# Optimization experiments

Hardware: AMD Instinct MI355X
Metric: run time of the kernel (lower is better)

Reference implementation:

```python
import jax, jax.numpy as jnp
import numpy as np

B, L, HID = 128, 256, 768
HID2 = 2 * HID
CDIM, SDIM, NPROJ = 192, 128, 128
FDIM = CDIM + SDIM + 1
BIG = 1e9  # finite pad so sorted invalid tokens go last without inf/nan issues


def setup_inputs() -> dict:
    key = jax.random.key(0)
    ks = jax.random.split(key, 12)
    H = jax.random.normal(ks[0], (B, L, HID), dtype=jnp.float32)
    tt = jax.random.randint(ks[1], (B, L), 0, 2, dtype=jnp.int32)
    m = jnp.ones((B, L), dtype=jnp.int32)
    s = 1.0 / np.sqrt(HID2)
    Wc = jax.random.uniform(ks[2], (CDIM, HID2), minval=-s, maxval=s, dtype=jnp.float32)
    bc = jax.random.uniform(ks[3], (CDIM,), minval=-s, maxval=s, dtype=jnp.float32)
    Ws = jax.random.uniform(ks[4], (SDIM, HID2), minval=-s, maxval=s, dtype=jnp.float32)
    bs = jax.random.uniform(ks[5], (SDIM,), minval=-s, maxval=s, dtype=jnp.float32)
    gate = jnp.array([0.5], dtype=jnp.float32)
    ln_g = jnp.ones((FDIM,), dtype=jnp.float32)
    ln_b = jnp.zeros((FDIM,), dtype=jnp.float32)
    sc = 1.0 / np.sqrt(FDIM)
    Wcls = jax.random.uniform(ks[6], (2, FDIM), minval=-sc, maxval=sc, dtype=jnp.float32)
    bcls = jax.random.uniform(ks[7], (2,), minval=-sc, maxval=sc, dtype=jnp.float32)
    d = jax.random.normal(ks[8], (NPROJ, HID), dtype=jnp.float32)
    proj_dirs = d / jnp.linalg.norm(d, axis=1, keepdims=True)
    return {"H": H, "tt": tt, "m": m, "Wc": Wc, "bc": bc, "Ws": Ws, "bs": bs,
            "gate": gate, "ln_g": ln_g, "ln_b": ln_b, "Wcls": Wcls, "bcls": bcls,
            "proj_dirs": proj_dirs}


def _forward(H, tt, m, Wc, bc, Ws, bs, gate, ln_g, ln_b, Wcls, bcls, proj_dirs):
    mask0 = (tt == 0) & (m == 1)  # [B,L]
    mask1 = (tt == 1) & (m == 1)
    f0 = mask0.astype(H.dtype)
    f1 = mask1.astype(H.dtype)
    cls = H[:, 0]  # [B,HID]
    mean0 = jnp.einsum('blh,bl->bh', H, f0) / jnp.clip(f0.sum(1, keepdims=True), 1.0)
    mean1 = jnp.einsum('blh,bl->bh', H, f1) / jnp.clip(f1.sum(1, keepdims=True), 1.0)
    rep = jnp.concatenate([cls, mean0 - mean1], axis=1)  # [B,2*HID]
    C = rep @ Wc.T + bc
    S = rep @ Ws.T + bs
    g = jax.nn.sigmoid(gate)  # [1]
    fused = jnp.concatenate([C * (1.0 - g), S * g], axis=1)

    # max-sliced W1 between token-type-0 and token-type-1 token sets, batched.
    P = jnp.einsum('blh,ph->blp', H, proj_dirs)  # [B,L,NPROJ]
    x0 = jnp.sort(jnp.where(mask0[..., None], P, BIG), axis=1)  # valid tokens first
    x1 = jnp.sort(jnp.where(mask1[..., None], P, BIG), axis=1)
    n0 = mask0.sum(1)
    n1 = mask1.sum(1)
    mcnt = jnp.minimum(n0, n1)  # [B]
    rmask = (jnp.arange(L)[None, :] < mcnt[:, None])[..., None]  # [B,L,1]
    diff = jnp.where(rmask, x0, 0.0) - jnp.where(rmask, x1, 0.0)
    mean_abs = jnp.abs(diff).sum(1) / jnp.maximum(mcnt, 1)[:, None].astype(P.dtype)  # [B,NPROJ]
    d_ot = mean_abs.max(axis=1, keepdims=True)  # [B,1]

    feat = jnp.concatenate([fused, d_ot], axis=1)  # [B,FDIM]
    mu = feat.mean(-1, keepdims=True)
    var = feat.var(-1, keepdims=True)
    normed = (feat - mu) * jax.lax.rsqrt(var + 1e-5) * ln_g + ln_b
    return normed @ Wcls.T + bcls  # [B,2]


def reference(H, tt, m, Wc, bc, Ws, bs, gate, ln_g, ln_b, Wcls, bcls, proj_dirs):
    return _forward(H, tt, m, Wc, bc, Ws, bs, gate, ln_g, ln_b, Wcls, bcls, proj_dirs)
```

## Files before the change

### kernel.cpp

```cpp
#include <hip/hip_runtime.h>
#include <cmath>

#define B_   128
#define L_   256
#define HID_ 768
#define HID2_ 1536
#define CDIM_ 192
#define SDIM_ 128
#define NPROJ_ 128
#define FDIM_ 321

typedef __attribute__((ext_vector_type(8))) short bf16x8;
typedef __attribute__((ext_vector_type(4))) float f32x4;

__device__ inline unsigned short bf_hi_trunc(float x) {
    return (unsigned short)(__float_as_uint(x) >> 16);
}
__device__ inline float bf2f(unsigned short s) {
    return __uint_as_float(((unsigned int)s) << 16);
}
__device__ inline unsigned short f2bf_rne(float x) {
    unsigned int u = __float_as_uint(x);
    unsigned int r = (u + 0x7fff + ((u >> 16) & 1)) >> 16;
    return (unsigned short)r;
}

__global__ __launch_bounds__(192) void stats_part(
    const float* __restrict__ H, const int* __restrict__ tt,
    const int* __restrict__ mm, float* __restrict__ part)
{
    int b  = blockIdx.x >> 2;
    int pr = blockIdx.x & 3;
    int tid = threadIdx.x;

    __shared__ float sf0[64], sf1[64];
    if (tid < 64) {
        int l = pr * 64 + tid;
        int t = tt[b * L_ + l];
        int mv = mm[b * L_ + l];
        sf0[tid] = (t == 0 && mv == 1) ? 1.f : 0.f;
        sf1[tid] = (t == 1 && mv == 1) ? 1.f : 0.f;
    }
    __syncthreads();

    const float* Hb = H + ((size_t)(b * L_ + pr * 64)) * HID_;
    float4 a0 = make_float4(0.f, 0.f, 0.f, 0.f);
    float4 a1 = make_float4(0.f, 0.f, 0.f, 0.f);
    for (int l = 0; l < 64; ++l) {
        float4 x = *(const float4*)(Hb + (size_t)l * HID_ + tid * 4);
        float f0 = sf0[l], f1 = sf1[l];
        a0.x += x.x * f0; a0.y += x.y * f0; a0.z += x.z * f0; a0.w += x.w * f0;
        a1.x += x.x * f1; a1.y += x.y * f1; a1.z += x.z * f1; a1.w += x.w * f1;
    }
    float* dst = part + ((size_t)(b * 4 + pr)) * HID2_;
    *(float4*)(dst + tid * 4) = a0;
    *(float4*)(dst + HID_ + tid * 4) = a1;
}

__global__ __launch_bounds__(256) void stats_fin(
    const float* __restrict__ H, const int* __restrict__ tt,
    const int* __restrict__ mm, const float* __restrict__ part,
    float* __restrict__ rep)
{
    int b = blockIdx.x;
    int tid = threadIdx.x;
    int t = tt[b * L_ + tid];
    int mv = mm[b * L_ + tid];
    int n0 = __syncthreads_count(t == 0 && mv == 1);
    int n1 = __syncthreads_count(t == 1 && mv == 1);
    float r0 = 1.f / fmaxf((float)n0, 1.f);
    float r1 = 1.f / fmaxf((float)n1, 1.f);

    const float* pp = part + (size_t)b * 4 * HID2_;
    for (int h = tid; h < HID_; h += 256) {
        float a0 = pp[h] + pp[HID2_ + h] + pp[2 * HID2_ + h] + pp[3 * HID2_ + h];
        float a1 = pp[HID_ + h] + pp[HID2_ + HID_ + h]
                 + pp[2 * HID2_ + HID_ + h] + pp[3 * HID2_ + HID_ + h];
        rep[(size_t)b * HID2_ + h] = H[(size_t)b * L_ * HID_ + h];
        rep[(size_t)b * HID2_ + HID_ + h] = a0 * r0 - a1 * r1;
    }
}

__global__ __launch_bounds__(256) void head_kernel(
    const float* __restrict__ rep, const float* __restrict__ Wc,
    const float* __restrict__ bc, const float* __restrict__ Ws,
    const float* __restrict__ bs, const float* __restrict__ gate,
    float* __restrict__ fused)
{
    int w = blockIdx.x * 4 + (threadIdx.x >> 6);
    int lane = threadIdx.x & 63;
    int b = w / (CDIM_ + SDIM_);
    int o = w % (CDIM_ + SDIM_);
    bool isC = (o < CDIM_);
    const float4* wr = (const float4*)(isC ? (Wc + (size_t)o * HID2_)
                                           : (Ws + (size_t)(o - CDIM_) * HID2_));
    const float4* rp = (const float4*)(rep + (size_t)b * HID2_);
    float acc = 0.f;
#pragma unroll
    for (int u = 0; u < 6; ++u) {
        int k4 = lane + u * 64;
        float4 a = rp[k4];
        float4 ww = wr[k4];
        acc += a.x * ww.x + a.y * ww.y + a.z * ww.z + a.w * ww.w;
    }
    for (int off = 32; off; off >>= 1) acc += __shfl_xor(acc, off, 64);
    if (lane == 0) {
        float g = 1.0f / (1.0f + expf(-gate[0]));
        float bias = isC ? bc[o] : bs[o - CDIM_];
        float scale = isC ? (1.0f - g) : g;
        fused[(size_t)b * (CDIM_ + SDIM_) + o] = (acc + bias) * scale;
    }
}

__global__ __launch_bounds__(256) void conv_proj(
    const float* __restrict__ Pd, unsigned short* __restrict__ hi,
    unsigned short* __restrict__ lo)
{
    int i = blockIdx.x * 256 + threadIdx.x;
    float4 v = ((const float4*)Pd)[i];
    ushort4 h, l;
    h.x = bf_hi_trunc(v.x); l.x = f2bf_rne(v.x - bf2f(h.x));
    h.y = bf_hi_trunc(v.y); l.y = f2bf_rne(v.y - bf2f(h.y));
    h.z = bf_hi_trunc(v.z); l.z = f2bf_rne(v.z - bf2f(h.z));
    h.w = bf_hi_trunc(v.w); l.w = f2bf_rne(v.w - bf2f(h.w));
    ((ushort4*)hi)[i] = h;
    ((ushort4*)lo)[i] = l;
}

#define LDSROW 72
__global__ __launch_bounds__(256) void gemm_mfma(
    const float* __restrict__ H, const unsigned short* __restrict__ Pjh,
    const unsigned short* __restrict__ Pjl, float* __restrict__ Pt)
{
    __shared__ unsigned short Ps[2][128 * LDSROW];
    __shared__ unsigned short Hs[2][64 * LDSROW];

    int tid = threadIdx.x;
    int w = tid >> 6;
    int lane = tid & 63;
    int c = lane & 15;
    int q = lane >> 4;

    int b = blockIdx.x >> 2;
    int lbase = (blockIdx.x & 3) * 64;

    const float* Hbase = H + ((size_t)(b * L_ + lbase)) * HID_;

    int hrow = tid >> 3;
    int hc4  = tid & 7;
    int prow = tid >> 2;
    int pk8  = tid & 3;

    f32x4 acc[2][4] = {};

    float4 hreg[2];
    uint4  phreg[2], plreg[2];

    hreg[0]  = *(const float4*)(Hbase + (size_t)hrow * HID_ + hc4 * 4);
    hreg[1]  = *(const float4*)(Hbase + (size_t)(hrow + 32) * HID_ + hc4 * 4);
    phreg[0] = *(const uint4*)(Pjh + (size_t)prow * HID_ + pk8 * 8);
    phreg[1] = *(const uint4*)(Pjh + (size_t)(prow + 64) * HID_ + pk8 * 8);
    plreg[0] = *(const uint4*)(Pjl + (size_t)prow * HID_ + pk8 * 8);
    plreg[1] = *(const uint4*)(Pjl + (size_t)(prow + 64) * HID_ + pk8 * 8);
#pragma unroll
    for (int u = 0; u < 2; ++u) {
        int row = hrow + u * 32;
        float4 v = hreg[u];
        ushort4 h, l;
        h.x = bf_hi_trunc(v.x); l.x = f2bf_rne(v.x - bf2f(h.x));
        h.y = bf_hi_trunc(v.y); l.y = f2bf_rne(v.y - bf2f(h.y));
        h.z = bf_hi_trunc(v.z); l.z = f2bf_rne(v.z - bf2f(h.z));
        h.w = bf_hi_trunc(v.w); l.w = f2bf_rne(v.w - bf2f(h.w));
        *(ushort4*)&Hs[0][row * LDSROW + hc4 * 4]      = h;
        *(ushort4*)&Hs[0][row * LDSROW + 32 + hc4 * 4] = l;
    }
#pragma unroll
    for (int u = 0; u < 2; ++u) {
        int row = prow + u * 64;
        *(uint4*)&Ps[0][row * LDSROW + pk8 * 8]      = phreg[u];
        *(uint4*)&Ps[0][row * LDSROW + 32 + pk8 * 8] = plreg[u];
    }
    __syncthreads();

    for (int it = 0; it < 24; ++it) {
        int cur = it & 1;
        int nxt = cur ^ 1;

        if (it + 1 < 24) {
            int k0 = (it + 1) * 32;
            hreg[0]  = *(const float4*)(Hbase + (size_t)hrow * HID_ + k0 + hc4 * 4);
            hreg[1]  = *(const float4*)(Hbase + (size_t)(hrow + 32) * HID_ + k0 + hc4 * 4);
            phreg[0] = *(const uint4*)(Pjh + (size_t)prow * HID_ + k0 + pk8 * 8);
            phreg[1] = *(const uint4*)(Pjh + (size_t)(prow + 64) * HID_ + k0 + pk8 * 8);
            plreg[0] = *(const uint4*)(Pjl + (size_t)prow * HID_ + k0 + pk8 * 8);
            plreg[1] = *(const uint4*)(Pjl + (size_t)(prow + 64) * HID_ + k0 + pk8 * 8);
        }

        bf16x8 ah[2], al[2], bh[4], bl[4];
#pragma unroll
        for (int pt = 0; pt < 2; ++pt) {
            int p = w * 32 + pt * 16 + c;
            ah[pt] = *(const bf16x8*)&Ps[cur][p * LDSROW + q * 8];
            al[pt] = *(const bf16x8*)&Ps[cur][p * LDSROW + 32 + q * 8];
        }
#pragma unroll
        for (int lt = 0; lt < 4; ++lt) {
            int l = lt * 16 + c;
            bh[lt] = *(const bf16x8*)&Hs[cur][l * LDSROW + q * 8];
            bl[lt] = *(const bf16x8*)&Hs[cur][l * LDSROW + 32 + q * 8];
        }
#pragma unroll
        for (int pt = 0; pt < 2; ++pt)
#pragma unroll
        for (int lt = 0; lt < 4; ++lt) {
            acc[pt][lt] = __builtin_amdgcn_mfma_f32_16x16x32_bf16(ah[pt], bh[lt], acc[pt][lt], 0, 0, 0);
            acc[pt][lt] = __builtin_amdgcn_mfma_f32_16x16x32_bf16(ah[pt], bl[lt], acc[pt][lt], 0, 0, 0);
            acc[pt][lt] = __builtin_amdgcn_mfma_f32_16x16x32_bf16(al[pt], bh[lt], acc[pt][lt], 0, 0, 0);
        }

        if (it + 1 < 24) {
#pragma unroll
            for (int u = 0; u < 2; ++u) {
                int row = hrow + u * 32;
                float4 v = hreg[u];
                ushort4 h, l;
                h.x = bf_hi_trunc(v.x); l.x = f2bf_rne(v.x - bf2f(h.x));
                h.y = bf_hi_trunc(v.y); l.y = f2bf_rne(v.y - bf2f(h.y));
                h.z = bf_hi_trunc(v.z); l.z = f2bf_rne(v.z - bf2f(h.z));
                h.w = bf_hi_trunc(v.w); l.w = f2bf_rne(v.w - bf2f(h.w));
                *(ushort4*)&Hs[nxt][row * LDSROW + hc4 * 4]      = h;
                *(ushort4*)&Hs[nxt][row * LDSROW + 32 + hc4 * 4] = l;
            }
#pragma unroll
            for (int u = 0; u < 2; ++u) {
                int row = prow + u * 64;
                *(uint4*)&Ps[nxt][row * LDSROW + pk8 * 8]      = phreg[u];
                *(uint4*)&Ps[nxt][row * LDSROW + 32 + pk8 * 8] = plreg[u];
            }
        }
        __syncthreads();
    }

#pragma unroll
    for (int pt = 0; pt < 2; ++pt)
#pragma unroll
    for (int lt = 0; lt < 4; ++lt)
#pragma unroll
    for (int r = 0; r < 4; ++r) {
        int p = w * 32 + pt * 16 + q * 4 + r;
        int l = lbase + lt * 16 + c;
        Pt[((size_t)(b * NPROJ_ + p)) * L_ + l] = acc[pt][lt][r];
    }
}

__device__ inline void bitonic256_u32(unsigned v[4], int lane)
{
    for (int k = 2; k <= 256; k <<= 1) {
        for (int j = k >> 1; j > 0; j >>= 1) {
            if (j >= 64) {
                int rj = j >> 6;
#pragma unroll
                for (int r = 0; r < 4; ++r) {
                    if ((r & rj) == 0) {
                        int i = (r << 6) | lane;
                        bool up = ((i & k) == 0);
                        unsigned lo = min(v[r], v[r | rj]);
                        unsigned hi = max(v[r], v[r | rj]);
                        v[r]      = up ? lo : hi;
                        v[r | rj] = up ? hi : lo;
                    }
                }
            } else {
#pragma unroll
                for (int r = 0; r < 4; ++r) {
                    int i = (r << 6) | lane;
                    unsigned w = (unsigned)__shfl_xor((int)v[r], j, 64);
                    bool lower = ((lane & j) == 0);
                    bool up = ((i & k) == 0);
                    v[r] = (lower == up) ? min(v[r], w) : max(v[r], w);
                }
            }
        }
    }
}

__global__ __launch_bounds__(256) void ot_kernel(
    const float* __restrict__ Pt, const int* __restrict__ tt,
    const int* __restrict__ mm, float* __restrict__ dist)
{
    int w = blockIdx.x * 4 + (threadIdx.x >> 6);
    int lane = threadIdx.x & 63;
    int b = w >> 7;
    int p = w & (NPROJ_ - 1);

    float4 pv = *(const float4*)(Pt + ((size_t)(b * NPROJ_ + p)) * L_ + lane * 4);
    int4 t4 = *(const int4*)(tt + (size_t)b * L_ + lane * 4);
    int4 m4 = *(const int4*)(mm + (size_t)b * L_ + lane * 4);

    float pvals[4] = {pv.x, pv.y, pv.z, pv.w};
    int tv[4] = {t4.x, t4.y, t4.z, t4.w};
    int mv[4] = {m4.x, m4.y, m4.z, m4.w};

    unsigned key[4];
#pragma unroll
    for (int r = 0; r < 4; ++r) {
        unsigned u = __float_as_uint(pvals[r]);
        unsigned s = (u & 0x80000000u) ? ~u : (u | 0x80000000u);
        unsigned label = (mv[r] == 1) ? (unsigned)tv[r] : 2u;
        key[r] = (s & ~3u) | label;
    }

    bitonic256_u32(key, lane);

    unsigned c[4];
    int lab[4];
    float tval[4];
#pragma unroll
    for (int r = 0; r < 4; ++r) {
        lab[r] = (int)(key[r] & 3u);
        unsigned s = key[r] & ~3u;
        unsigned u = (s & 0x80000000u) ? (s ^ 0x80000000u) : ~s;
        tval[r] = __uint_as_float(u);
        c[r] = ((lab[r] == 0) ? 0x10000u : 0u) | ((lab[r] == 1) ? 1u : 0u);
#pragma unroll
        for (int d = 1; d < 64; d <<= 1) {
            unsigned t = (unsigned)__shfl_up((int)c[r], d, 64);
            if (lane >= d) c[r] += t;
        }
    }
    unsigned tot[4];
#pragma unroll
    for (int r = 0; r < 4; ++r) tot[r] = (unsigned)__shfl((int)c[r], 63, 64);
    unsigned total = tot[0] + tot[1] + tot[2] + tot[3];
    int n0 = (int)(total >> 16), n1 = (int)(total & 0xffffu);
    int m = (n0 < n1) ? n0 : n1;

    float ssum = 0.f;
    unsigned run = 0;
#pragma unroll
    for (int r = 0; r < 4; ++r) {
        unsigned C = c[r] + run;
        int c0 = (int)(C >> 16), c1 = (int)(C & 0xffffu);
        int s0 = (lab[r] == 0), s1 = (lab[r] == 1);
        int wi = abs(min(c0, m) - min(c1, m));
        int wp = abs(min(c0 - s0, m) - min(c1 - s1, m));
        ssum += tval[r] * (float)(wp - wi);
        run += tot[r];
    }
    for (int off = 32; off; off >>= 1) ssum += __shfl_xor(ssum, off, 64);
    if (lane == 0) dist[b * NPROJ_ + p] = ssum / (float)((m > 1) ? m : 1);
}

__global__ __launch_bounds__(64) void final_kernel(
    const float* __restrict__ fused, const float* __restrict__ dist,
    const float* __restrict__ ln_g, const float* __restrict__ ln_b,
    const float* __restrict__ Wcls, const float* __restrict__ bcls,
    float* __restrict__ out)
{
    int b = blockIdx.x;
    int lane = threadIdx.x;

    float mx = fmaxf(dist[b * NPROJ_ + lane], dist[b * NPROJ_ + 64 + lane]);
    for (int off = 32; off; off >>= 1) mx = fmaxf(mx, __shfl_xor(mx, off, 64));

    float fv[6];
    float sum = 0.f, sq = 0.f;
#pragma unroll
    for (int u = 0; u < 6; ++u) {
        int j = lane + u * 64;
        float x = 0.f;
        if (j < CDIM_ + SDIM_) x = fused[(size_t)b * (CDIM_ + SDIM_) + j];
        else if (j == CDIM_ + SDIM_) x = mx;
        fv[u] = x;
        if (j < FDIM_) { sum += x; sq += x * x; }
    }
    for (int off = 32; off; off >>= 1) {
        sum += __shfl_xor(sum, off, 64);
        sq  += __shfl_xor(sq,  off, 64);
    }
    float mu = sum / (float)FDIM_;
    float var = sq / (float)FDIM_ - mu * mu;
    float inv = rsqrtf(var + 1e-5f);

    float d0 = 0.f, d1 = 0.f;
#pragma unroll
    for (int u = 0; u < 6; ++u) {
        int j = lane + u * 64;
        if (j < FDIM_) {
            float nx = (fv[u] - mu) * inv * ln_g[j] + ln_b[j];
            d0 += nx * Wcls[j];
            d1 += nx * Wcls[FDIM_ + j];
        }
    }
    for (int off = 32; off; off >>= 1) {
        d0 += __shfl_xor(d0, off, 64);
        d1 += __shfl_xor(d1, off, 64);
    }
    if (lane == 0) {
        out[b * 2 + 0] = d0 + bcls[0];
        out[b * 2 + 1] = d1 + bcls[1];
    }
}

extern "C" void kernel_launch(void* const* d_in, const int* in_sizes, int n_in,
                              void* d_out, int out_size, void* d_ws, size_t ws_size,
                              hipStream_t stream)
{
    const float* H    = (const float*)d_in[0];
    const int*   tt   = (const int*)d_in[1];
    const int*   mm   = (const int*)d_in[2];
    const float* Wc   = (const float*)d_in[3];
    const float* bc   = (const float*)d_in[4];
    const float* Ws   = (const float*)d_in[5];
    const float* bs   = (const float*)d_in[6];
    const float* gate = (const float*)d_in[7];
    const float* ln_g = (const float*)d_in[8];
    const float* ln_b = (const float*)d_in[9];
    const float* Wcls = (const float*)d_in[10];
    const float* bcls = (const float*)d_in[11];
    const float* Pd   = (const float*)d_in[12];
    float* out = (float*)d_out;

    float* ws = (float*)d_ws;
    float* Pt    = ws;
    float* part  = Pt;
    float* rep   = Pt + (size_t)B_ * NPROJ_ * L_;
    float* fused = rep + (size_t)B_ * HID2_;
    float* dist  = fused + (size_t)B_ * (CDIM_ + SDIM_);
    unsigned short* Pjh = (unsigned short*)(dist + (size_t)B_ * NPROJ_);
    unsigned short* Pjl = Pjh + (size_t)NPROJ_ * HID_;

    conv_proj<<<NPROJ_ * HID_ / 4 / 256, 256, 0, stream>>>(Pd, Pjh, Pjl);
    stats_part<<<B_ * 4, 192, 0, stream>>>(H, tt, mm, part);
    stats_fin<<<B_, 256, 0, stream>>>(H, tt, mm, part, rep);
    head_kernel<<<B_ * (CDIM_ + SDIM_) / 4, 256, 0, stream>>>(rep, Wc, bc, Ws, bs, gate, fused);
    gemm_mfma<<<B_ * 4, 256, 0, stream>>>(H, Pjh, Pjl, Pt);
    ot_kernel<<<B_ * NPROJ_ / 4, 256, 0, stream>>>(Pt, tt, mm, dist);
    final_kernel<<<B_, 64, 0, stream>>>(fused, dist, ln_g, ln_b, Wcls, bcls, out);
}
```

Measured before the change: 265.4 us.

## Reorder bitonic sort to lane-major keys and use a single wave scan

The OT kernel now treats each lane's four keys as consecutive sorted positions. The bitonic stages with stride below four become in-register compare-exchanges instead of cross-lane shuffles. The four per-register prefix scans are replaced by one serial in-lane sum plus a single wave-wide scan, which cuts shuffle and instruction count. Separately, the masked-mean partial reduction is split into eight token chunks per batch instead of four, giving more blocks in exchange for a larger reduction in stats_fin.

```diff
diff --git a/kernel.cpp b/kernel.cpp
--- a/kernel.cpp
+++ b/kernel.cpp
@@ -29,13 +29,13 @@
     const float* __restrict__ H, const int* __restrict__ tt,
     const int* __restrict__ mm, float* __restrict__ part)
 {
-    int b  = blockIdx.x >> 2;
-    int pr = blockIdx.x & 3;
+    int b  = blockIdx.x >> 3;
+    int pr = blockIdx.x & 7;
     int tid = threadIdx.x;
 
-    __shared__ float sf0[64], sf1[64];
-    if (tid < 64) {
-        int l = pr * 64 + tid;
+    __shared__ float sf0[32], sf1[32];
+    if (tid < 32) {
+        int l = pr * 32 + tid;
         int t = tt[b * L_ + l];
         int mv = mm[b * L_ + l];
         sf0[tid] = (t == 0 && mv == 1) ? 1.f : 0.f;
@@ -43,16 +43,16 @@
     }
     __syncthreads();
 
-    const float* Hb = H + ((size_t)(b * L_ + pr * 64)) * HID_;
+    const float* Hb = H + ((size_t)(b * L_ + pr * 32)) * HID_;
     float4 a0 = make_float4(0.f, 0.f, 0.f, 0.f);
     float4 a1 = make_float4(0.f, 0.f, 0.f, 0.f);
-    for (int l = 0; l < 64; ++l) {
+    for (int l = 0; l < 32; ++l) {
         float4 x = *(const float4*)(Hb + (size_t)l * HID_ + tid * 4);
         float f0 = sf0[l], f1 = sf1[l];
         a0.x += x.x * f0; a0.y += x.y * f0; a0.z += x.z * f0; a0.w += x.w * f0;
         a1.x += x.x * f1; a1.y += x.y * f1; a1.z += x.z * f1; a1.w += x.w * f1;
     }
-    float* dst = part + ((size_t)(b * 4 + pr)) * HID2_;
+    float* dst = part + ((size_t)(b * 8 + pr)) * HID2_;
     *(float4*)(dst + tid * 4) = a0;
     *(float4*)(dst + HID_ + tid * 4) = a1;
 }
@@ -71,11 +71,14 @@
     float r0 = 1.f / fmaxf((float)n0, 1.f);
     float r1 = 1.f / fmaxf((float)n1, 1.f);
 
-    const float* pp = part + (size_t)b * 4 * HID2_;
+    const float* pp = part + (size_t)b * 8 * HID2_;
     for (int h = tid; h < HID_; h += 256) {
-        float a0 = pp[h] + pp[HID2_ + h] + pp[2 * HID2_ + h] + pp[3 * HID2_ + h];
-        float a1 = pp[HID_ + h] + pp[HID2_ + HID_ + h]
-                 + pp[2 * HID2_ + HID_ + h] + pp[3 * HID2_ + HID_ + h];
+        float a0 = 0.f, a1 = 0.f;
+#pragma unroll
+        for (int q = 0; q < 8; ++q) {
+            a0 += pp[(size_t)q * HID2_ + h];
+            a1 += pp[(size_t)q * HID2_ + HID_ + h];
+        }
         rep[(size_t)b * HID2_ + h] = H[(size_t)b * L_ * HID_ + h];
         rep[(size_t)b * HID2_ + HID_ + h] = a0 * r0 - a1 * r1;
     }
@@ -253,37 +256,6 @@
     }
 }
 
-__device__ inline void bitonic256_u32(unsigned v[4], int lane)
-{
-    for (int k = 2; k <= 256; k <<= 1) {
-        for (int j = k >> 1; j > 0; j >>= 1) {
-            if (j >= 64) {
-                int rj = j >> 6;
-#pragma unroll
-                for (int r = 0; r < 4; ++r) {
-                    if ((r & rj) == 0) {
-                        int i = (r << 6) | lane;
-                        bool up = ((i & k) == 0);
-                        unsigned lo = min(v[r], v[r | rj]);
-                        unsigned hi = max(v[r], v[r | rj]);
-                        v[r]      = up ? lo : hi;
-                        v[r | rj] = up ? hi : lo;
-                    }
-                }
-            } else {
-#pragma unroll
-                for (int r = 0; r < 4; ++r) {
-                    int i = (r << 6) | lane;
-                    unsigned w = (unsigned)__shfl_xor((int)v[r], j, 64);
-                    bool lower = ((lane & j) == 0);
-                    bool up = ((i & k) == 0);
-                    v[r] = (lower == up) ? min(v[r], w) : max(v[r], w);
-                }
-            }
-        }
-    }
-}
-
 __global__ __launch_bounds__(256) void ot_kernel(
     const float* __restrict__ Pt, const int* __restrict__ tt,
     const int* __restrict__ mm, float* __restrict__ dist)
@@ -310,42 +282,77 @@
         key[r] = (s & ~3u) | label;
     }
 
-    bitonic256_u32(key, lane);
-
-    unsigned c[4];
+    {
+        unsigned mn0 = min(key[0], key[1]), mx0 = max(key[0], key[1]);
+        key[0] = mn0; key[1] = mx0;
+        unsigned mn1 = min(key[2], key[3]), mx1 = max(key[2], key[3]);
+        key[2] = mx1; key[3] = mn1;
+    }
+#pragma unroll
+    for (int k = 4; k <= 256; k <<= 1) {
+        bool up = (lane & (k >> 2)) == 0;
+#pragma unroll
+        for (int j = k >> 1; j >= 4; j >>= 1) {
+            int lj = j >> 2;
+            bool lower_eq_up;
+            {
+            }
+#pragma unroll
+            for (int r = 0; r < 4; ++r) {
+                unsigned o = (unsigned)__shfl_xor((int)key[r], lj, 64);
+                bool lower = (lane & lj) == 0;
+                unsigned mn = min(key[r], o), mx = max(key[r], o);
+                key[r] = (lower == up) ? mn : mx;
+            }
+        }
+        {
+            unsigned mn0 = min(key[0], key[2]), mx0 = max(key[0], key[2]);
+            key[0] = up ? mn0 : mx0; key[2] = up ? mx0 : mn0;
+            unsigned mn1 = min(key[1], key[3]), mx1 = max(key[1], key[3]);
+            key[1] = up ? mn1 : mx1; key[3] = up ? mx1 : mn1;
+        }
+        {
+            unsigned mn0 = min(key[0], key[1]), mx0 = max(key[0], key[1]);
+            key[0] = up ? mn0 : mx0; key[1] = up ? mx0 : mn0;
+            unsigned mn1 = min(key[2], key[3]), mx1 = max(key[2], key[3]);
+            key[2] = up ? mn1 : mx1; key[3] = up ? mx1 : mn1;
+        }
+    }
+
     int lab[4];
     float tval[4];
+    unsigned sincl[4];
+    unsigned run = 0;
 #pragma unroll
     for (int r = 0; r < 4; ++r) {
         lab[r] = (int)(key[r] & 3u);
         unsigned s = key[r] & ~3u;
         unsigned u = (s & 0x80000000u) ? (s ^ 0x80000000u) : ~s;
         tval[r] = __uint_as_float(u);
-        c[r] = ((lab[r] == 0) ? 0x10000u : 0u) | ((lab[r] == 1) ? 1u : 0u);
-#pragma unroll
-        for (int d = 1; d < 64; d <<= 1) {
-            unsigned t = (unsigned)__shfl_up((int)c[r], d, 64);
-            if (lane >= d) c[r] += t;
-        }
-    }
-    unsigned tot[4];
-#pragma unroll
-    for (int r = 0; r < 4; ++r) tot[r] = (unsigned)__shfl((int)c[r], 63, 64);
-    unsigned total = tot[0] + tot[1] + tot[2] + tot[3];
+        unsigned unit = ((lab[r] == 0) ? 0x10000u : 0u) | ((lab[r] == 1) ? 1u : 0u);
+        run += unit;
+        sincl[r] = run;
+    }
+    unsigned inc = run;
+#pragma unroll
+    for (int d = 1; d < 64; d <<= 1) {
+        unsigned t = (unsigned)__shfl_up((int)inc, d, 64);
+        if (lane >= d) inc += t;
+    }
+    unsigned ex = inc - run;
+    unsigned total = (unsigned)__shfl((int)inc, 63, 64);
     int n0 = (int)(total >> 16), n1 = (int)(total & 0xffffu);
     int m = (n0 < n1) ? n0 : n1;
 
     float ssum = 0.f;
-    unsigned run = 0;
 #pragma unroll
     for (int r = 0; r < 4; ++r) {
-        unsigned C = c[r] + run;
+        unsigned C = ex + sincl[r];
         int c0 = (int)(C >> 16), c1 = (int)(C & 0xffffu);
         int s0 = (lab[r] == 0), s1 = (lab[r] == 1);
         int wi = abs(min(c0, m) - min(c1, m));
         int wp = abs(min(c0 - s0, m) - min(c1 - s1, m));
         ssum += tval[r] * (float)(wp - wi);
-        run += tot[r];
     }
     for (int off = 32; off; off >>= 1) ssum += __shfl_xor(ssum, off, 64);
     if (lane == 0) dist[b * NPROJ_ + p] = ssum / (float)((m > 1) ? m : 1);
@@ -431,7 +438,7 @@
     unsigned short* Pjl = Pjh + (size_t)NPROJ_ * HID_;
 
     conv_proj<<<NPROJ_ * HID_ / 4 / 256, 256, 0, stream>>>(Pd, Pjh, Pjl);
-    stats_part<<<B_ * 4, 192, 0, stream>>>(H, tt, mm, part);
+    stats_part<<<B_ * 8, 192, 0, stream>>>(H, tt, mm, part);
     stats_fin<<<B_, 256, 0, stream>>>(H, tt, mm, part, rep);
     head_kernel<<<B_ * (CDIM_ + SDIM_) / 4, 256, 0, stream>>>(rep, Wc, bc, Ws, bs, gate, fused);
     gemm_mfma<<<B_ * 4, 256, 0, stream>>>(H, Pjh, Pjl, Pt);
```

New measurement: 252.8 us. 1.05x faster.
